# Optimization experiments

Measured on AMD Instinct MI355X. Metric: run time of the kernel, lower is better.

Reference implementation:

```python
import jax, jax.numpy as jnp
import numpy as np
from jax import lax

B = 32768
L = 200          # window_size
K = 5            # conv kernel
CIN = 6
FLAT = L - K + 1  # 196, conv1d valid output length (out channels = 1)


def setup_inputs() -> dict:
    key = jax.random.key(0)
    ks = jax.random.split(key, 9)
    s = lambda *sh: 1.0 / np.sqrt(sh[-1])
    x = jax.random.normal(ks[0], (B, CIN, L), dtype=jnp.float32)
    conv_w = jax.random.normal(ks[1], (1, CIN, K), dtype=jnp.float32) * (1.0 / np.sqrt(CIN * K))
    conv_b = jax.random.normal(ks[2], (1,), dtype=jnp.float32) * 0.1
    w1 = jax.random.normal(ks[3], (FLAT, 50), dtype=jnp.float32) * (1.0 / np.sqrt(FLAT))
    b1 = jax.random.normal(ks[4], (50,), dtype=jnp.float32) * 0.1
    w2 = jax.random.normal(ks[5], (50, 30), dtype=jnp.float32) * (1.0 / np.sqrt(50))
    b2 = jax.random.normal(ks[6], (30,), dtype=jnp.float32) * 0.1
    w3 = jax.random.normal(ks[7], (30, 15), dtype=jnp.float32) * (1.0 / np.sqrt(30))
    b3 = jax.random.normal(ks[8], (15,), dtype=jnp.float32) * 0.1
    return {"x": x, "conv_w": conv_w, "conv_b": conv_b, "w1": w1, "b1": b1,
            "w2": w2, "b2": b2, "w3": w3, "b3": b3}


def reference(x, conv_w, conv_b, w1, b1, w2, b2, w3, b3):
    # conv1d (valid): [B,6,200] -> [B,1,196]
    y = lax.conv_general_dilated(x, conv_w, window_strides=(1,), padding='VALID',
                                 dimension_numbers=('NCH', 'OIH', 'NCH'))
    y = y + conv_b[None, :, None]
    h = y.reshape(x.shape[0], -1)                       # [B,196]
    h = jax.nn.relu(h @ w1 + b1)                        # [B,50]
    h = jax.nn.relu(h @ w2 + b2)                        # [B,30]
    out = h @ w3 + b3                                   # [B,15]
    # Procrustes orthogonalization of the 3x3 block
    R = out[:, :9].reshape(-1, 3, 3)
    U, _, VT = jnp.linalg.svd(R)                        # batched 3x3 SVD
    det = jnp.linalg.det(jnp.matmul(U, VT))             # [B]
    scale = jnp.stack([jnp.ones_like(det), jnp.ones_like(det), det], axis=1)  # diag(1,1,det)
    R_norm = jnp.matmul(U, VT * scale[:, :, None])      # U @ S @ VT
    return jnp.concatenate([R_norm.reshape(-1, 9), out[:, 9:]], axis=1)
```

## Files before the change

kernel.cpp:

```cpp
#include <hip/hip_runtime.h>
#include <math.h>

#define BATCH 32768
#define LW    200
#define CIN   6
#define KSZ   5
#define FLAT  196
#define NH1   50
#define NH2   30
#define NOUT  15


template<int NS, int TB, int NLD, int TW, int NSPLIT>
__device__ __forceinline__ void conv_fc1_body(
    const float* __restrict__ x,
    const float* __restrict__ cw, const float* __restrict__ cb,
    const float* __restrict__ w1,
    float* __restrict__ part,
    float* __restrict__ tile)
{
    const int lane = threadIdx.x;
    const int bid  = blockIdx.x;
    const int r = bid & 7;
    const int q = bid >> 3;
    const int g = r * 64 + q / NSPLIT;
    const int s = q - (q / NSPLIT) * NSPLIT;

    const int kstart = NS * s;
    const int tbase  = TB * s;
    const int off    = kstart - tbase;

    float w[CIN][KSZ];
#pragma unroll
    for (int c = 0; c < CIN; ++c)
#pragma unroll
        for (int k = 0; k < KSZ; ++k)
            w[c][k] = __int_as_float(
                __builtin_amdgcn_readfirstlane(__float_as_int(cw[c * KSZ + k])));
    const float bias = __int_as_float(
        __builtin_amdgcn_readfirstlane(__float_as_int(cb[0])));

    int goff[NLD];
    int loff[NLD];
#pragma unroll
    for (int u = 0; u < NLD; ++u) {
        int g4  = lane + 64 * u;
        int row = g4 / NLD;
        int c4  = g4 - row * NLD;
        goff[u] = row * (CIN * LW) + 4 * c4;
        loff[u] = row * TW + 4 * c4;
    }
    const float* xw = x + (size_t)g * 64 * (CIN * LW) + tbase;

    float acc[NS];
#pragma unroll
    for (int i = 0; i < NS; ++i) acc[i] = bias;

    float4 buf[NLD];
#pragma unroll
    for (int u = 0; u < NLD; ++u)
        buf[u] = *(const float4*)(xw + goff[u]);

#pragma unroll
    for (int ch = 0; ch < CIN; ++ch) {
#pragma unroll
        for (int u = 0; u < NLD; ++u) {
            float* dst = tile + loff[u];
            dst[0] = buf[u].x; dst[1] = buf[u].y; dst[2] = buf[u].z; dst[3] = buf[u].w;
        }
        if (ch + 1 < CIN) {
#pragma unroll
            for (int u = 0; u < NLD; ++u)
                buf[u] = *(const float4*)(xw + (ch + 1) * LW + goff[u]);
        }
        const float* row = tile + lane * TW + off;
        float x0 = row[0], x1 = row[1], x2 = row[2], x3 = row[3];
#pragma unroll
        for (int i = 0; i < NS; ++i) {
            float x4v = row[i + 4];
            float a = acc[i];
            a = fmaf(x0, w[ch][0], a);
            a = fmaf(x1, w[ch][1], a);
            a = fmaf(x2, w[ch][2], a);
            a = fmaf(x3, w[ch][3], a);
            a = fmaf(x4v, w[ch][4], a);
            acc[i] = a;
            x0 = x1; x1 = x2; x2 = x3; x3 = x4v;
        }
    }

    float h1p[NH1];
#pragma unroll
    for (int j = 0; j < NH1; ++j) h1p[j] = 0.f;
#pragma unroll
    for (int ii = 0; ii < NS; ++ii) {
        const float* wrow = w1 + (size_t)(kstart + ii) * NH1;
        float c = acc[ii];
#pragma unroll
        for (int j = 0; j < NH1; ++j) h1p[j] = fmaf(c, wrow[j], h1p[j]);
    }

    float* pb = part + (size_t)(s * NH1) * BATCH + (size_t)g * 64 + lane;
#pragma unroll
    for (int j = 0; j < NH1; ++j)
        pb[(size_t)j * BATCH] = h1p[j];
}

__global__ void __launch_bounds__(64) __attribute__((amdgpu_waves_per_eu(4, 4)))
conv_fc1_k7(const float* __restrict__ x,
            const float* __restrict__ cw, const float* __restrict__ cb,
            const float* __restrict__ w1, float* __restrict__ part)
{
    __shared__ float tile[64 * 33];
    conv_fc1_body<28, 28, 8, 33, 7>(x, cw, cb, w1, part, tile);
}

__global__ void __launch_bounds__(64) __attribute__((amdgpu_waves_per_eu(2, 2)))
conv_fc1_k4(const float* __restrict__ x,
            const float* __restrict__ cw, const float* __restrict__ cb,
            const float* __restrict__ w1, float* __restrict__ part)
{
    __shared__ float tile[64 * 57];
    conv_fc1_body<49, 48, 14, 57, 4>(x, cw, cb, w1, part, tile);
}

__global__ void __launch_bounds__(64) __attribute__((amdgpu_waves_per_eu(1, 1)))
conv_fc1_k2(const float* __restrict__ x,
            const float* __restrict__ cw, const float* __restrict__ cb,
            const float* __restrict__ w1, float* __restrict__ part)
{
    __shared__ float tile[64 * 105];
    conv_fc1_body<98, 96, 26, 105, 2>(x, cw, cb, w1, part, tile);
}

template<int NSPLIT>
__global__ void __launch_bounds__(64) __attribute__((amdgpu_waves_per_eu(2, 4)))
tail_kernel(
    const float* __restrict__ part,
    const float* __restrict__ b1,
    const float* __restrict__ w2, const float* __restrict__ b2,
    const float* __restrict__ w3, const float* __restrict__ b3,
    float* __restrict__ out)
{
    const int bid = blockIdx.x;
    const int g   = (bid & 7) * 64 + (bid >> 3);
    const int b   = g * 64 + threadIdx.x;

    float h1[NH1];
#pragma unroll
    for (int j = 0; j < NH1; ++j) {
        float a = b1[j];
#pragma unroll
        for (int s = 0; s < NSPLIT; ++s)
            a += part[(size_t)(s * NH1 + j) * BATCH + b];
        h1[j] = fmaxf(a, 0.f);
    }

    float h2[NH2];
#pragma unroll
    for (int j = 0; j < NH2; ++j) h2[j] = b2[j];
#pragma unroll
    for (int k = 0; k < NH1; ++k) {
        float hk = h1[k];
        const float* row = w2 + k * NH2;
#pragma unroll
        for (int j = 0; j < NH2; ++j) h2[j] = fmaf(hk, row[j], h2[j]);
    }
#pragma unroll
    for (int j = 0; j < NH2; ++j) h2[j] = fmaxf(h2[j], 0.f);

    float o[NOUT];
#pragma unroll
    for (int j = 0; j < NOUT; ++j) o[j] = b3[j];
#pragma unroll
    for (int k = 0; k < NH2; ++k) {
        float hk = h2[k];
        const float* row = w3 + k * NOUT;
#pragma unroll
        for (int j = 0; j < NOUT; ++j) o[j] = fmaf(hk, row[j], o[j]);
    }

    float r00 = o[0], r01 = o[1], r02 = o[2];
    float r10 = o[3], r11 = o[4], r12 = o[5];
    float r20 = o[6], r21 = o[7], r22 = o[8];

    float A[4][4], V[4][4];
    A[0][0] = r00 + r11 + r22;
    A[1][1] = r00 - r11 - r22;
    A[2][2] = r11 - r00 - r22;
    A[3][3] = r22 - r00 - r11;
    A[0][1] = A[1][0] = r21 - r12;
    A[0][2] = A[2][0] = r02 - r20;
    A[0][3] = A[3][0] = r10 - r01;
    A[1][2] = A[2][1] = r01 + r10;
    A[1][3] = A[3][1] = r02 + r20;
    A[2][3] = A[3][2] = r12 + r21;
#pragma unroll
    for (int i = 0; i < 4; ++i)
#pragma unroll
        for (int j = 0; j < 4; ++j) V[i][j] = (i == j) ? 1.f : 0.f;

    const int pr[6][2] = {{0,1},{0,2},{0,3},{1,2},{1,3},{2,3}};
    for (int sweep = 0; sweep < 7; ++sweep) {
#pragma unroll
        for (int pi = 0; pi < 6; ++pi) {
            const int p = pr[pi][0], qq = pr[pi][1];
            float apq = A[p][qq];
            if (fabsf(apq) > 1e-20f) {
                float theta = (A[qq][qq] - A[p][p]) / (2.f * apq);
                float t = copysignf(1.f, theta) / (fabsf(theta) + sqrtf(1.f + theta * theta));
                float c = rsqrtf(1.f + t * t);
                float sn = t * c;
#pragma unroll
                for (int k = 0; k < 4; ++k) {
                    float akp = A[k][p], akq = A[k][qq];
                    A[k][p] = c * akp - sn * akq;
                    A[k][qq] = sn * akp + c * akq;
                }
#pragma unroll
                for (int k = 0; k < 4; ++k) {
                    float apk = A[p][k], aqk = A[qq][k];
                    A[p][k] = c * apk - sn * aqk;
                    A[qq][k] = sn * apk + c * aqk;
                }
#pragma unroll
                for (int k = 0; k < 4; ++k) {
                    float vkp = V[k][p], vkq = V[k][qq];
                    V[k][p] = c * vkp - sn * vkq;
                    V[k][qq] = sn * vkp + c * vkq;
                }
            }
        }
    }

    int best = 0;
    float bl = A[0][0];
#pragma unroll
    for (int i = 1; i < 4; ++i)
        if (A[i][i] > bl) { bl = A[i][i]; best = i; }

    float vsel[4];
#pragma unroll
    for (int k = 0; k < 4; ++k) {
        float v = V[k][0];
        v = (best == 1) ? V[k][1] : v;
        v = (best == 2) ? V[k][2] : v;
        v = (best == 3) ? V[k][3] : v;
        vsel[k] = v;
    }
    float vw = vsel[0], vx = vsel[1], vy = vsel[2], vz = vsel[3];
    float inv = rsqrtf(vw * vw + vx * vx + vy * vy + vz * vz);
    vw *= inv; vx *= inv; vy *= inv; vz *= inv;

    float xx = vx * vx, yy = vy * vy, zz = vz * vz;
    float xy = vx * vy, xz = vx * vz, yz = vy * vz;
    float wx = vw * vx, wy = vw * vy, wz = vw * vz;

    float* ob = out + (long)b * NOUT;
    ob[0]  = 1.f - 2.f * (yy + zz);
    ob[1]  = 2.f * (xy - wz);
    ob[2]  = 2.f * (xz + wy);
    ob[3]  = 2.f * (xy + wz);
    ob[4]  = 1.f - 2.f * (xx + zz);
    ob[5]  = 2.f * (yz - wx);
    ob[6]  = 2.f * (xz - wy);
    ob[7]  = 2.f * (yz + wx);
    ob[8]  = 1.f - 2.f * (xx + yy);
    ob[9]  = o[9];
    ob[10] = o[10];
    ob[11] = o[11];
    ob[12] = o[12];
    ob[13] = o[13];
    ob[14] = o[14];
}

extern "C" void kernel_launch(void* const* d_in, const int* in_sizes, int n_in,
                              void* d_out, int out_size, void* d_ws, size_t ws_size,
                              hipStream_t stream) {
    const float* x  = (const float*)d_in[0];
    const float* cw = (const float*)d_in[1];
    const float* cb = (const float*)d_in[2];
    const float* w1 = (const float*)d_in[3];
    const float* b1 = (const float*)d_in[4];
    const float* w2 = (const float*)d_in[5];
    const float* b2 = (const float*)d_in[6];
    const float* w3 = (const float*)d_in[7];
    const float* b3 = (const float*)d_in[8];
    float* outp = (float*)d_out;
    float* part = (float*)d_ws;

    const size_t need7 = (size_t)7 * NH1 * BATCH * sizeof(float);
    const size_t need4 = (size_t)4 * NH1 * BATCH * sizeof(float);

    if (ws_size >= need7) {
        conv_fc1_k7<<<7 * (BATCH / 64), 64, 0, stream>>>(x, cw, cb, w1, part);
        tail_kernel<7><<<BATCH / 64, 64, 0, stream>>>(part, b1, w2, b2, w3, b3, outp);
    } else if (ws_size >= need4) {
        conv_fc1_k4<<<4 * (BATCH / 64), 64, 0, stream>>>(x, cw, cb, w1, part);
        tail_kernel<4><<<BATCH / 64, 64, 0, stream>>>(part, b1, w2, b2, w3, b3, outp);
    } else {
        conv_fc1_k2<<<2 * (BATCH / 64), 64, 0, stream>>>(x, cw, cb, w1, part);
        tail_kernel<2><<<BATCH / 64, 64, 0, stream>>>(part, b1, w2, b2, w3, b3, outp);
    }
}
```

Baseline: 346.5 us.

## Rework conv_fc1_k7 loads, split FC1 into halves, drop waves_per_eu hints

conv_fc1_k7 is rewritten as a standalone kernel that loads 64 sample rows as two 32-row halves into shared memory, so each lane does fewer float4 loads in flight. The FC1 partial product is now done in two 25-column halves in every conv kernel, which cuts live registers. The amdgpu_waves_per_eu attributes are removed from all kernels, and the tail kernel streams the h1 sums straight into the h2 accumulation instead of keeping a 50-element h1 array. Together these target register pressure and occupancy, at the risk of extra serialization and shared-memory round trips in k7.

```diff
diff --git a/kernel.cpp b/kernel.cpp
--- a/kernel.cpp
+++ b/kernel.cpp
@@ -9,14 +9,117 @@
 #define NH1   50
 #define NH2   30
 #define NOUT  15
-
+#define XROW  (CIN * LW)
+
+
+__global__ void __launch_bounds__(64)
+conv_fc1_k7(const float* __restrict__ x,
+            const float* __restrict__ cw, const float* __restrict__ cb,
+            const float* __restrict__ w1, float* __restrict__ part)
+{
+    __shared__ float tile[64 * 33];
+
+    const int lane = threadIdx.x;
+    const int bid  = blockIdx.x;
+    const int r  = bid & 7;
+    const int q  = bid >> 3;
+    const int gq = q / 7;
+    const int s  = q - gq * 7;
+    const int g  = r * 64 + gq;
+    const int kstart = 28 * s;
+
+    float w[CIN][KSZ];
+#pragma unroll
+    for (int c = 0; c < CIN; ++c)
+#pragma unroll
+        for (int k = 0; k < KSZ; ++k)
+            w[c][k] = __int_as_float(
+                __builtin_amdgcn_readfirstlane(__float_as_int(cw[c * KSZ + k])));
+    const float bias = __int_as_float(
+        __builtin_amdgcn_readfirstlane(__float_as_int(cb[0])));
+
+    int goff[4];
+    int loff[4];
+#pragma unroll
+    for (int u = 0; u < 4; ++u) {
+        int g4  = lane + 64 * u;
+        int row = g4 >> 3;
+        int c4  = g4 & 7;
+        goff[u] = row * XROW + 4 * c4;
+        loff[u] = row * 33 + 4 * c4;
+    }
+    const float* xw = x + (size_t)g * 64 * XROW + kstart;
+
+    float acc[28];
+#pragma unroll
+    for (int i = 0; i < 28; ++i) acc[i] = bias;
+
+    float4 buf[4];
+#pragma unroll
+    for (int u = 0; u < 4; ++u)
+        buf[u] = *(const float4*)(xw + goff[u]);
+
+#pragma unroll
+    for (int ch = 0; ch < CIN; ++ch) {
+#pragma unroll
+        for (int u = 0; u < 4; ++u) {
+            float* dst = tile + loff[u];
+            dst[0] = buf[u].x; dst[1] = buf[u].y; dst[2] = buf[u].z; dst[3] = buf[u].w;
+        }
+#pragma unroll
+        for (int u = 0; u < 4; ++u)
+            buf[u] = *(const float4*)(xw + ch * LW + 32 * XROW + goff[u]);
+#pragma unroll
+        for (int u = 0; u < 4; ++u) {
+            float* dst = tile + 32 * 33 + loff[u];
+            dst[0] = buf[u].x; dst[1] = buf[u].y; dst[2] = buf[u].z; dst[3] = buf[u].w;
+        }
+        if (ch + 1 < CIN) {
+#pragma unroll
+            for (int u = 0; u < 4; ++u)
+                buf[u] = *(const float4*)(xw + (ch + 1) * LW + goff[u]);
+        }
+        const float* row = tile + lane * 33;
+        float x0 = row[0], x1 = row[1], x2 = row[2], x3 = row[3];
+#pragma unroll
+        for (int i = 0; i < 28; ++i) {
+            float x4v = row[i + 4];
+            float a = acc[i];
+            a = fmaf(x0, w[ch][0], a);
+            a = fmaf(x1, w[ch][1], a);
+            a = fmaf(x2, w[ch][2], a);
+            a = fmaf(x3, w[ch][3], a);
+            a = fmaf(x4v, w[ch][4], a);
+            acc[i] = a;
+            x0 = x1; x1 = x2; x2 = x3; x3 = x4v;
+        }
+    }
+
+    float* pb = part + (size_t)(s * NH1) * BATCH + (size_t)g * 64 + lane;
+#pragma unroll
+    for (int half = 0; half < 2; ++half) {
+        const int j0 = half * 25;
+        float h1p[25];
+#pragma unroll
+        for (int j = 0; j < 25; ++j) h1p[j] = 0.f;
+#pragma unroll
+        for (int ii = 0; ii < 28; ++ii) {
+            const float* wrow = w1 + (size_t)(kstart + ii) * NH1 + j0;
+            float c = acc[ii];
+#pragma unroll
+            for (int j = 0; j < 25; ++j) h1p[j] = fmaf(c, wrow[j], h1p[j]);
+        }
+#pragma unroll
+        for (int j = 0; j < 25; ++j)
+            pb[(size_t)(j0 + j) * BATCH] = h1p[j];
+    }
+}
 
 template<int NS, int TB, int NLD, int TW, int NSPLIT>
 __device__ __forceinline__ void conv_fc1_body(
     const float* __restrict__ x,
     const float* __restrict__ cw, const float* __restrict__ cb,
-    const float* __restrict__ w1,
-    float* __restrict__ part,
+    const float* __restrict__ w1, float* __restrict__ part,
     float* __restrict__ tile)
 {
     const int lane = threadIdx.x;
@@ -25,7 +128,6 @@
     const int q = bid >> 3;
     const int g = r * 64 + q / NSPLIT;
     const int s = q - (q / NSPLIT) * NSPLIT;
-
     const int kstart = NS * s;
     const int tbase  = TB * s;
     const int off    = kstart - tbase;
@@ -40,17 +142,16 @@
     const float bias = __int_as_float(
         __builtin_amdgcn_readfirstlane(__float_as_int(cb[0])));
 
-    int goff[NLD];
-    int loff[NLD];
+    int goff[NLD], loff[NLD];
 #pragma unroll
     for (int u = 0; u < NLD; ++u) {
         int g4  = lane + 64 * u;
         int row = g4 / NLD;
         int c4  = g4 - row * NLD;
-        goff[u] = row * (CIN * LW) + 4 * c4;
+        goff[u] = row * XROW + 4 * c4;
         loff[u] = row * TW + 4 * c4;
     }
-    const float* xw = x + (size_t)g * 64 * (CIN * LW) + tbase;
+    const float* xw = x + (size_t)g * 64 * XROW + tbase;
 
     float acc[NS];
 #pragma unroll
@@ -58,8 +159,7 @@
 
     float4 buf[NLD];
 #pragma unroll
-    for (int u = 0; u < NLD; ++u)
-        buf[u] = *(const float4*)(xw + goff[u]);
+    for (int u = 0; u < NLD; ++u) buf[u] = *(const float4*)(xw + goff[u]);
 
 #pragma unroll
     for (int ch = 0; ch < CIN; ++ch) {
@@ -89,33 +189,27 @@
         }
     }
 
-    float h1p[NH1];
-#pragma unroll
-    for (int j = 0; j < NH1; ++j) h1p[j] = 0.f;
-#pragma unroll
-    for (int ii = 0; ii < NS; ++ii) {
-        const float* wrow = w1 + (size_t)(kstart + ii) * NH1;
-        float c = acc[ii];
-#pragma unroll
-        for (int j = 0; j < NH1; ++j) h1p[j] = fmaf(c, wrow[j], h1p[j]);
-    }
-
     float* pb = part + (size_t)(s * NH1) * BATCH + (size_t)g * 64 + lane;
 #pragma unroll
-    for (int j = 0; j < NH1; ++j)
-        pb[(size_t)j * BATCH] = h1p[j];
-}
-
-__global__ void __launch_bounds__(64) __attribute__((amdgpu_waves_per_eu(4, 4)))
-conv_fc1_k7(const float* __restrict__ x,
-            const float* __restrict__ cw, const float* __restrict__ cb,
-            const float* __restrict__ w1, float* __restrict__ part)
-{
-    __shared__ float tile[64 * 33];
-    conv_fc1_body<28, 28, 8, 33, 7>(x, cw, cb, w1, part, tile);
-}
-
-__global__ void __launch_bounds__(64) __attribute__((amdgpu_waves_per_eu(2, 2)))
+    for (int half = 0; half < 2; ++half) {
+        const int j0 = half * 25;
+        float h1p[25];
+#pragma unroll
+        for (int j = 0; j < 25; ++j) h1p[j] = 0.f;
+#pragma unroll
+        for (int ii = 0; ii < NS; ++ii) {
+            const float* wrow = w1 + (size_t)(kstart + ii) * NH1 + j0;
+            float c = acc[ii];
+#pragma unroll
+            for (int j = 0; j < 25; ++j) h1p[j] = fmaf(c, wrow[j], h1p[j]);
+        }
+#pragma unroll
+        for (int j = 0; j < 25; ++j)
+            pb[(size_t)(j0 + j) * BATCH] = h1p[j];
+    }
+}
+
+__global__ void __launch_bounds__(64)
 conv_fc1_k4(const float* __restrict__ x,
             const float* __restrict__ cw, const float* __restrict__ cb,
             const float* __restrict__ w1, float* __restrict__ part)
@@ -124,7 +218,7 @@
     conv_fc1_body<49, 48, 14, 57, 4>(x, cw, cb, w1, part, tile);
 }
 
-__global__ void __launch_bounds__(64) __attribute__((amdgpu_waves_per_eu(1, 1)))
+__global__ void __launch_bounds__(64)
 conv_fc1_k2(const float* __restrict__ x,
             const float* __restrict__ cw, const float* __restrict__ cb,
             const float* __restrict__ w1, float* __restrict__ part)
@@ -134,7 +228,7 @@
 }
 
 template<int NSPLIT>
-__global__ void __launch_bounds__(64) __attribute__((amdgpu_waves_per_eu(2, 4)))
+__global__ void __launch_bounds__(64)
 tail_kernel(
     const float* __restrict__ part,
     const float* __restrict__ b1,
@@ -145,23 +239,19 @@
     const int bid = blockIdx.x;
     const int g   = (bid & 7) * 64 + (bid >> 3);
     const int b   = g * 64 + threadIdx.x;
-
-    float h1[NH1];
-#pragma unroll
-    for (int j = 0; j < NH1; ++j) {
-        float a = b1[j];
+    const float* pb = part + b;
+
+    float h2[NH2];
+#pragma unroll
+    for (int j = 0; j < NH2; ++j) h2[j] = b2[j];
+
+#pragma unroll
+    for (int k = 0; k < NH1; ++k) {
+        float a = b1[k];
 #pragma unroll
         for (int s = 0; s < NSPLIT; ++s)
-            a += part[(size_t)(s * NH1 + j) * BATCH + b];
-        h1[j] = fmaxf(a, 0.f);
-    }
-
-    float h2[NH2];
-#pragma unroll
-    for (int j = 0; j < NH2; ++j) h2[j] = b2[j];
-#pragma unroll
-    for (int k = 0; k < NH1; ++k) {
-        float hk = h1[k];
+            a += pb[(size_t)(s * NH1 + k) * BATCH];
+        float hk = fmaxf(a, 0.f);
         const float* row = w2 + k * NH2;
 #pragma unroll
         for (int j = 0; j < NH2; ++j) h2[j] = fmaf(hk, row[j], h2[j]);
```

Measured after the change: 331.4 us. 4.4% less time.
